# Kernel optimization log

Measured on AMD Instinct MI355X. Metric: run time of the kernel, lower is better.

The kernel has to match this reference:

```python
import jax, jax.numpy as jnp
import numpy as np

KH = KW = 3
K = KH * KW
GROUPS = 8


def conv_same(x, w, b=None):
    out = jax.lax.conv_general_dilated(x, w, (1, 1), 'SAME',
                                       dimension_numbers=('NHWC', 'HWIO', 'NHWC'))
    if b is not None:
        out = out + b
    return out


def feature_selection(x, w_att, w_sel):
    pooled = x.mean(axis=(1, 2), keepdims=True)            # [B,1,1,C]
    attn = jax.nn.sigmoid(conv_same(pooled, w_att))        # 1x1 conv, sigmoid
    return conv_same(x * (attn + 1.0), w_sel)              # [B,H,W,F]


def deform_sample(x, sy, sx):
    # x: [H,W,G,Cg]; sy,sx: [H,W,G,K] fractional sample coords (zero outside)
    H, W, G, _ = x.shape
    y0 = jnp.floor(sy)
    x0 = jnp.floor(sx)
    wy1 = sy - y0
    wx1 = sx - x0
    gi = jnp.arange(G)[None, None, :, None]

    def gather(yi, xi):
        valid = (yi >= 0) & (yi <= H - 1) & (xi >= 0) & (xi <= W - 1)
        yc = jnp.clip(yi, 0, H - 1).astype(jnp.int32)
        xc = jnp.clip(xi, 0, W - 1).astype(jnp.int32)
        v = x[yc, xc, gi]                                   # [H,W,G,K,Cg]
        return v * valid[..., None]

    v00 = gather(y0, x0)
    v01 = gather(y0, x0 + 1)
    v10 = gather(y0 + 1, x0)
    v11 = gather(y0 + 1, x0 + 1)
    wy1 = wy1[..., None]
    wx1 = wx1[..., None]
    top = v00 * (1 - wx1) + v01 * wx1
    bot = v10 * (1 - wx1) + v11 * wx1
    return top * (1 - wy1) + bot * wy1                      # [H,W,G,K,Cg]


def dcnv2(x, align, w_om, b_om, w_dcn, b_dcn):
    # x: [B,H,W,C] input to deform-conv; align: [B,H,W,Ca] alignment feature
    B, H, W, C = x.shape
    G = GROUPS
    Cg = C // G
    om = conv_same(align, w_om, b_om)                       # [B,H,W,G*3*K]
    off = om[..., :G * 2 * K].reshape(B, H, W, G, K, 2)     # (dy, dx)
    mask = jax.nn.sigmoid(om[..., G * 2 * K:]).reshape(B, H, W, G, K)

    iy = jnp.arange(H, dtype=x.dtype)[:, None, None, None]
    ix = jnp.arange(W, dtype=x.dtype)[None, :, None, None]
    ky, kx = jnp.meshgrid(jnp.arange(KH) - (KH - 1) // 2,
                          jnp.arange(KW) - (KW - 1) // 2, indexing='ij')
    ky = ky.reshape(K).astype(x.dtype)
    kx = kx.reshape(K).astype(x.dtype)
    sy = iy + ky + off[..., 0]                              # [B,H,W,G,K]
    sx = ix + kx + off[..., 1]

    xg = x.reshape(B, H, W, G, Cg)
    sampled = jax.vmap(deform_sample)(xg, sy, sx)           # [B,H,W,G,K,Cg]
    sampled = sampled * mask[..., None]
    sampled = sampled.transpose(0, 1, 2, 4, 3, 5).reshape(B, H, W, K, C)
    wk = w_dcn.reshape(K, C, -1)                            # [K,C,F]
    return jnp.einsum('bhwkc,kcf->bhwf', sampled, wk) + b_dcn


def reference(coarse, fine, w_att, w_sel, w_off, w_om, b_om, w_dcn, b_dcn):
    B, H, W, _ = fine.shape
    coarse_up = jax.image.resize(coarse, (B, H, W, coarse.shape[-1]), 'bilinear')
    fine_cal = feature_selection(fine, w_att, w_sel)
    fc = jnp.concatenate([fine_cal, coarse_up * 2.0], axis=-1)
    align = conv_same(fc, w_off)                            # 1x1, no bias
    aligned = jax.nn.relu(dcnv2(coarse_up, align, w_om, b_om, w_dcn, b_dcn))
    return aligned + fine_cal


def setup_inputs() -> dict:
    key = jax.random.key(0)
    ks = jax.random.split(key, 8)
    B, H, W = 4, 64, 64
    Cc, Cf, F = 256, 256, 256
    s = lambda fan: (2.0 / fan) ** 0.5
    return {
        'coarse': jax.random.normal(ks[0], (B, H // 2, W // 2, Cc), jnp.float32),
        'fine': jax.random.normal(ks[1], (B, H, W, Cf), jnp.float32),
        'w_att': jax.random.normal(ks[2], (1, 1, Cf, Cf), jnp.float32) * s(Cf),
        'w_sel': jax.random.normal(ks[3], (1, 1, Cf, F), jnp.float32) * s(Cf),
        'w_off': jax.random.normal(ks[4], (1, 1, F + Cc, 2 * F), jnp.float32) * s(F + Cc),
        'w_om': jax.random.normal(ks[5], (3, 3, 2 * F, GROUPS * 3 * K), jnp.float32) * 0.01,
        'b_om': jnp.zeros((GROUPS * 3 * K,), jnp.float32),
        'w_dcn': jax.random.normal(ks[6], (3, 3, Cc, F), jnp.float32) * s(9 * Cc),
        'b_dcn': jnp.zeros((F,), jnp.float32),
    }
```

## Files before the change

kernel.cpp:

```cpp
#include <hip/hip_runtime.h>
#include <hip/hip_bf16.h>
#include <cstddef>

constexpr int HWP = 64 * 64;
constexpr int CCH = 256;
constexpr int OMC = 216;
constexpr int KDC = 2304;

typedef __attribute__((ext_vector_type(8))) short bf16x8;
typedef __attribute__((ext_vector_type(4))) float f32x4;

__device__ inline unsigned short f2bf(float x) {
  __hip_bfloat16 h = __float2bfloat16(x);
  return *reinterpret_cast<unsigned short*>(&h);
}
__device__ inline float bf2f(unsigned short u) {
  unsigned int v = ((unsigned int)u) << 16;
  return __uint_as_float(v);
}
__device__ inline void bfpair(unsigned int u, float& a, float& b) {
  a = __uint_as_float(u << 16);
  b = __uint_as_float(u & 0xffff0000u);
}

__global__ __launch_bounds__(256) void prep_weights(
    const float* __restrict__ w_off, const float* __restrict__ w_om,
    const float* __restrict__ w_sel, const float* __restrict__ w_dcn,
    unsigned short* __restrict__ w_offT, unsigned short* __restrict__ w_omT,
    unsigned short* __restrict__ w_selT, unsigned short* __restrict__ w_dcnT) {
  int i = blockIdx.x * 256 + threadIdx.x;
  if (i < 512 * 512) {
    int n = i >> 9, k = i & 511;
    w_offT[i] = f2bf(w_off[k * 512 + n]);
  }
  if (i < 9 * 256 * 512) {
    int c = i & 511;
    int r = i >> 9;
    int tap = r >> 8;
    int n = r & 255;
    w_omT[i] = f2bf(n < OMC ? w_om[((size_t)tap * 512 + c) * OMC + n] : 0.f);
  }
  if (i < 256 * 256) {
    int n = i >> 8, k = i & 255;
    w_selT[i] = f2bf(w_sel[k * 256 + n]);
  }
  if (i < 9 * 256 * 256) {
    int tap = i >> 16, f = (i >> 8) & 255, c = i & 255;
    w_dcnT[i] = f2bf(w_dcn[((size_t)tap * 256 + c) * 256 + f]);
  }
}

__global__ __launch_bounds__(256) void pool_partial(
    const float* __restrict__ fine, float* __restrict__ partial) {
  int r = blockIdx.x;
  int b = blockIdx.y;
  int t = threadIdx.x;
  const float* src = fine + ((size_t)b * 4096 + r * 64) * 256 + t;
  float s = 0.f;
#pragma unroll 8
  for (int p = 0; p < 64; ++p) s += src[(size_t)p * 256];
  partial[((size_t)b * 64 + r) * 256 + t] = s;
}

__global__ __launch_bounds__(256) void pool_finish(
    const float* __restrict__ partial, const float* __restrict__ w_att,
    float* __restrict__ scale) {
  __shared__ float pl[256];
  int b = blockIdx.x;
  int t = threadIdx.x;
  const float* pp = partial + (size_t)b * 64 * 256 + t;
  float s = 0.f;
#pragma unroll 8
  for (int r = 0; r < 64; ++r) s += pp[(size_t)r * 256];
  pl[t] = s * (1.0f / 4096.0f);
  __syncthreads();
  float acc = 0.f;
  for (int ci = 0; ci < 256; ++ci) acc += pl[ci] * w_att[ci * 256 + t];
  scale[b * 256 + t] = 1.0f + 1.0f / (1.0f + expf(-acc));
}

__global__ __launch_bounds__(256) void upsample_kernel(
    const float* __restrict__ coarse, unsigned short* __restrict__ upbf,
    unsigned short* __restrict__ alignA) {
  int m = blockIdx.x;
  int c = threadIdx.x;
  int b = m >> 12, h = (m >> 6) & 63, w = m & 63;
  float cy = fminf(fmaxf(h * 0.5f - 0.25f, 0.f), 31.f);
  float cx = fminf(fmaxf(w * 0.5f - 0.25f, 0.f), 31.f);
  int y0 = (int)cy, x0 = (int)cx;
  float fy = cy - y0, fx = cx - x0;
  int y1 = min(y0 + 1, 31), x1 = min(x0 + 1, 31);
  const float* base = coarse + (size_t)b * 32 * 32 * CCH;
  float v00 = base[(y0 * 32 + x0) * CCH + c];
  float v01 = base[(y0 * 32 + x1) * CCH + c];
  float v10 = base[(y1 * 32 + x0) * CCH + c];
  float v11 = base[(y1 * 32 + x1) * CCH + c];
  float top = v00 + (v01 - v00) * fx;
  float bot = v10 + (v11 - v10) * fx;
  float v = top + (bot - top) * fy;
  upbf[(size_t)m * CCH + c] = f2bf(v);
  alignA[(size_t)m * 512 + 256 + c] = f2bf(2.f * v);
}

__global__ __launch_bounds__(256) void gemm_finecal_mfma(
    const float* __restrict__ fine, const float* __restrict__ scale,
    const unsigned short* __restrict__ w_selT,
    float* __restrict__ finecal, unsigned short* __restrict__ alignA) {
  __shared__ unsigned short As[128][72];
  __shared__ unsigned short Bs[64][72];
  __shared__ float sc[256];
  int n0 = blockIdx.x * 64;
  int m0 = blockIdx.y * 128;
  int t = threadIdx.x;
  int wid = t >> 6, lane = t & 63;
  int lrow = lane & 15, lq = lane >> 4;
  int bb = m0 >> 12;
  sc[t] = scale[bb * 256 + t];
  f32x4 acc[2][4];
#pragma unroll
  for (int i = 0; i < 2; ++i)
#pragma unroll
    for (int j = 0; j < 4; ++j) acc[i][j] = (f32x4){0.f, 0.f, 0.f, 0.f};
  for (int k0 = 0; k0 < 256; k0 += 64) {
    __syncthreads();
    for (int u = t; u < 128 * 8; u += 256) {
      int row = u >> 3, ck = u & 7;
      const float* fp = &fine[(size_t)(m0 + row) * 256 + k0 + ck * 8];
      float4 f0 = *(const float4*)fp;
      float4 f1 = *(const float4*)(fp + 4);
      int kb = k0 + ck * 8;
      ushort4 u0 = make_ushort4(f2bf(f0.x * sc[kb]), f2bf(f0.y * sc[kb + 1]),
                                f2bf(f0.z * sc[kb + 2]), f2bf(f0.w * sc[kb + 3]));
      ushort4 u1 = make_ushort4(f2bf(f1.x * sc[kb + 4]), f2bf(f1.y * sc[kb + 5]),
                                f2bf(f1.z * sc[kb + 6]), f2bf(f1.w * sc[kb + 7]));
      *(ushort4*)&As[row][ck * 8] = u0;
      *(ushort4*)&As[row][ck * 8 + 4] = u1;
    }
    for (int u = t; u < 64 * 8; u += 256) {
      int row = u >> 3, ck = u & 7;
      *(uint4*)&Bs[row][ck * 8] = *(const uint4*)&w_selT[(size_t)(n0 + row) * 256 + k0 + ck * 8];
    }
    __syncthreads();
#pragma unroll
    for (int kk = 0; kk < 2; ++kk) {
      bf16x8 a[2], b[4];
#pragma unroll
      for (int mt = 0; mt < 2; ++mt)
        a[mt] = *(const bf16x8*)&As[wid * 32 + mt * 16 + lrow][kk * 32 + lq * 8];
#pragma unroll
      for (int nt = 0; nt < 4; ++nt)
        b[nt] = *(const bf16x8*)&Bs[nt * 16 + lrow][kk * 32 + lq * 8];
#pragma unroll
      for (int mt = 0; mt < 2; ++mt)
#pragma unroll
        for (int nt = 0; nt < 4; ++nt)
          acc[mt][nt] = __builtin_amdgcn_mfma_f32_16x16x32_bf16(
              a[mt], b[nt], acc[mt][nt], 0, 0, 0);
    }
  }
#pragma unroll
  for (int mt = 0; mt < 2; ++mt)
#pragma unroll
    for (int nt = 0; nt < 4; ++nt)
#pragma unroll
      for (int r = 0; r < 4; ++r) {
        int m = m0 + wid * 32 + mt * 16 + lq * 4 + r;
        int n = n0 + nt * 16 + lrow;
        finecal[(size_t)m * 256 + n] = acc[mt][nt][r];
        alignA[(size_t)m * 512 + n] = f2bf(acc[mt][nt][r]);
      }
}

__global__ __launch_bounds__(256) void gemm_align_mfma(
    const unsigned short* __restrict__ alignA,
    const unsigned short* __restrict__ w_offT,
    unsigned short* __restrict__ alignBf) {
  __shared__ unsigned short As[128][72];
  __shared__ unsigned short Bs[64][72];
  int n0 = blockIdx.x * 64;
  int m0 = blockIdx.y * 128;
  int t = threadIdx.x;
  int wid = t >> 6, lane = t & 63;
  int lrow = lane & 15, lq = lane >> 4;
  f32x4 acc[2][4];
#pragma unroll
  for (int i = 0; i < 2; ++i)
#pragma unroll
    for (int j = 0; j < 4; ++j) acc[i][j] = (f32x4){0.f, 0.f, 0.f, 0.f};
  for (int k0 = 0; k0 < 512; k0 += 64) {
    __syncthreads();
    for (int u = t; u < 128 * 8; u += 256) {
      int row = u >> 3, ck = u & 7;
      *(uint4*)&As[row][ck * 8] =
          *(const uint4*)&alignA[(size_t)(m0 + row) * 512 + k0 + ck * 8];
    }
    for (int u = t; u < 64 * 8; u += 256) {
      int row = u >> 3, ck = u & 7;
      *(uint4*)&Bs[row][ck * 8] =
          *(const uint4*)&w_offT[(size_t)(n0 + row) * 512 + k0 + ck * 8];
    }
    __syncthreads();
#pragma unroll
    for (int kk = 0; kk < 2; ++kk) {
      bf16x8 a[2], b[4];
#pragma unroll
      for (int mt = 0; mt < 2; ++mt)
        a[mt] = *(const bf16x8*)&As[wid * 32 + mt * 16 + lrow][kk * 32 + lq * 8];
#pragma unroll
      for (int nt = 0; nt < 4; ++nt)
        b[nt] = *(const bf16x8*)&Bs[nt * 16 + lrow][kk * 32 + lq * 8];
#pragma unroll
      for (int mt = 0; mt < 2; ++mt)
#pragma unroll
        for (int nt = 0; nt < 4; ++nt)
          acc[mt][nt] = __builtin_amdgcn_mfma_f32_16x16x32_bf16(
              a[mt], b[nt], acc[mt][nt], 0, 0, 0);
    }
  }
#pragma unroll
  for (int mt = 0; mt < 2; ++mt)
#pragma unroll
    for (int nt = 0; nt < 4; ++nt)
#pragma unroll
      for (int r = 0; r < 4; ++r) {
        int m = m0 + wid * 32 + mt * 16 + lq * 4 + r;
        int n = n0 + nt * 16 + lrow;
        alignBf[(size_t)m * 512 + n] = f2bf(acc[mt][nt][r]);
      }
}

__global__ __launch_bounds__(256) void om_conv_mfma(
    const unsigned short* __restrict__ alignBf,
    const unsigned short* __restrict__ w_omT,
    const float* __restrict__ b_om,
    float* __restrict__ om) {
  __shared__ unsigned short As[4][66][72];
  __shared__ unsigned short Bs[2][64][72];
  int nblk = blockIdx.x;
  int mblk = blockIdx.y;
  int b = mblk >> 5, hp = mblk & 31;
  int h0 = hp * 2;
  int n0 = nblk * 64;
  int t = threadIdx.x;
  int wid = t >> 6, lane = t & 63;
  int wy = wid >> 1, wx = wid & 1;
  int lrow = lane & 15, lq = lane >> 4;
  const size_t imgbase = (size_t)b * 4096;
  f32x4 acc[4][2];
#pragma unroll
  for (int i = 0; i < 4; ++i)
#pragma unroll
    for (int j = 0; j < 2; ++j) acc[i][j] = (f32x4){0.f, 0.f, 0.f, 0.f};

  auto stageB = [&](int buf, int tap, int c0) {
    for (int u = t; u < 64 * 8; u += 256) {
      int n = u >> 3, ck = u & 7;
      *(uint4*)&Bs[buf][n][ck * 8] =
          *(const uint4*)&w_omT[((size_t)tap * 256 + n0 + n) * 512 + c0 * 64 + ck * 8];
    }
  };
  auto stageA = [&](int c0) {
    for (int u = t; u < 4 * 66 * 8; u += 256) {
      int dy = u / 528;
      int r = u - dy * 528;
      int px = r >> 3, ck = r & 7;
      int w = px - 1;
      int y = h0 - 1 + dy;
      uint4 v = make_uint4(0u, 0u, 0u, 0u);
      if (w >= 0 && w < 64 && y >= 0 && y < 64)
        v = *(const uint4*)&alignBf[(imgbase + y * 64 + w) * 512 + c0 * 64 + ck * 8];
      *(uint4*)&As[dy][px][ck * 8] = v;
    }
  };

  stageB(0, 0, 0);
  stageA(0);
  __syncthreads();
  int buf = 0;
  for (int c0 = 0; c0 < 8; ++c0) {
    for (int tap = 0; tap < 9; ++tap) {
      int ntap = tap + 1, nc0 = c0;
      if (ntap == 9) { ntap = 0; nc0 = (c0 + 1) & 7; }
      stageB(buf ^ 1, ntap, nc0);
      int dyt = tap / 3, dxt = tap - dyt * 3;
#pragma unroll
      for (int kk = 0; kk < 2; ++kk) {
        bf16x8 a[4], bb[2];
#pragma unroll
        for (int mt = 0; mt < 4; ++mt)
          a[mt] = *(const bf16x8*)&As[wy + dyt][mt * 16 + lrow + dxt][kk * 32 + lq * 8];
#pragma unroll
        for (int nt = 0; nt < 2; ++nt)
          bb[nt] = *(const bf16x8*)&Bs[buf][wx * 32 + nt * 16 + lrow][kk * 32 + lq * 8];
#pragma unroll
        for (int mt = 0; mt < 4; ++mt)
#pragma unroll
          for (int nt = 0; nt < 2; ++nt)
            acc[mt][nt] = __builtin_amdgcn_mfma_f32_16x16x32_bf16(
                a[mt], bb[nt], acc[mt][nt], 0, 0, 0);
      }
      __syncthreads();
      buf ^= 1;
    }
    if (c0 < 7) {
      stageA(c0 + 1);
      __syncthreads();
    }
  }
#pragma unroll
  for (int nt = 0; nt < 2; ++nt) {
    int n = n0 + wx * 32 + nt * 16 + lrow;
    if (n < OMC) {
      float bias = b_om[n];
#pragma unroll
      for (int mt = 0; mt < 4; ++mt) {
#pragma unroll
        for (int r = 0; r < 4; ++r) {
          size_t m = imgbase + (size_t)(h0 + wy) * 64 + mt * 16 + lq * 4 + r;
          om[m * OMC + n] = acc[mt][nt][r] + bias;
        }
      }
    }
  }
}

__global__ __launch_bounds__(256) void dcn_sample(
    const float* __restrict__ om, const unsigned short* __restrict__ upbf,
    unsigned short* __restrict__ S, int bh0) {
  __shared__ int offsA[256][4];
  __shared__ float wtsA[256][4];
  int blk = blockIdx.x;
  int bh = bh0 + (blk >> 1);
  int half = blk & 1;
  int b = bh >> 6, h = bh & 63;
  int p0 = half * 32;
  int m0g = bh * 64 + p0;
  int mloc0 = (bh - bh0) * 64 + p0;
  int t = threadIdx.x;
  const unsigned short* upb = upbf + (size_t)b * HWP * CCH;
  int lane = t & 63;
  int ph = t >> 6;
  int c = lane * 4;
  int g = lane >> 3;
  for (int tap = 0; tap < 9; ++tap) {
    int ky = tap / 3, kx = tap - ky * 3;
    __syncthreads();
    {
      int p = t >> 3, gg = t & 7;
      const float* omr = om + (size_t)(m0g + p) * OMC;
      float dy = omr[gg * 18 + tap * 2];
      float dx = omr[gg * 18 + tap * 2 + 1];
      float mk = 1.0f / (1.0f + expf(-omr[144 + gg * 9 + tap]));
      float sy = (float)(h + ky - 1) + dy;
      float sx = (float)(p0 + p + kx - 1) + dx;
      float y0f = floorf(sy), x0f = floorf(sx);
      float fy = sy - y0f, fx = sx - x0f;
      int y0 = (int)y0f, x0 = (int)x0f;
      int y1 = y0 + 1, x1 = x0 + 1;
      float vy0 = (y0 >= 0 && y0 <= 63) ? 1.f : 0.f;
      float vy1 = (y1 >= 0 && y1 <= 63) ? 1.f : 0.f;
      float vx0 = (x0 >= 0 && x0 <= 63) ? 1.f : 0.f;
      float vx1 = (x1 >= 0 && x1 <= 63) ? 1.f : 0.f;
      int yc0 = min(max(y0, 0), 63), yc1 = min(max(y1, 0), 63);
      int xc0 = min(max(x0, 0), 63), xc1 = min(max(x1, 0), 63);
      offsA[t][0] = (yc0 * 64 + xc0) * 256;
      offsA[t][1] = (yc0 * 64 + xc1) * 256;
      offsA[t][2] = (yc1 * 64 + xc0) * 256;
      offsA[t][3] = (yc1 * 64 + xc1) * 256;
      wtsA[t][0] = (1.f - fy) * (1.f - fx) * vy0 * vx0 * mk;
      wtsA[t][1] = (1.f - fy) * fx * vy0 * vx1 * mk;
      wtsA[t][2] = fy * (1.f - fx) * vy1 * vx0 * mk;
      wtsA[t][3] = fy * fx * vy1 * vx1 * mk;
    }
    __syncthreads();
#pragma unroll
    for (int pp = 0; pp < 8; ++pp) {
      int p = ph * 8 + pp;
      int idx = (p << 3) | g;
      int4 o = *(const int4*)&offsA[idx][0];
      float4 wv = *(const float4*)&wtsA[idx][0];
      uint2 u00 = *(const uint2*)&upb[o.x + c];
      uint2 u01 = *(const uint2*)&upb[o.y + c];
      uint2 u10 = *(const uint2*)&upb[o.z + c];
      uint2 u11 = *(const uint2*)&upb[o.w + c];
      float a0, a1, a2, a3, b0, b1, b2, b3, c0, c1, c2, c3, d0, d1, d2, d3;
      bfpair(u00.x, a0, a1); bfpair(u00.y, a2, a3);
      bfpair(u01.x, b0, b1); bfpair(u01.y, b2, b3);
      bfpair(u10.x, c0, c1); bfpair(u10.y, c2, c3);
      bfpair(u11.x, d0, d1); bfpair(u11.y, d2, d3);
      float v0 = wv.x * a0 + wv.y * b0 + wv.z * c0 + wv.w * d0;
      float v1 = wv.x * a1 + wv.y * b1 + wv.z * c1 + wv.w * d1;
      float v2 = wv.x * a2 + wv.y * b2 + wv.z * c2 + wv.w * d2;
      float v3 = wv.x * a3 + wv.y * b3 + wv.z * c3 + wv.w * d3;
      uint2 outv;
      outv.x = (unsigned int)f2bf(v0) | ((unsigned int)f2bf(v1) << 16);
      outv.y = (unsigned int)f2bf(v2) | ((unsigned int)f2bf(v3) << 16);
      *(uint2*)&S[(size_t)(mloc0 + p) * KDC + tap * 256 + c] = outv;
    }
  }
}

__global__ __launch_bounds__(256) void dcn_gemm(
    const unsigned short* __restrict__ S,
    const unsigned short* __restrict__ w_dcnT,
    const float* __restrict__ b_dcn,
    const float* __restrict__ finecal,
    float* __restrict__ outp, int m_base) {
  __shared__ unsigned short As[128][72];
  __shared__ unsigned short Bs[128][72];
  int n0 = blockIdx.x * 128;
  int mloc0 = blockIdx.y * 128;
  int m0 = m_base + mloc0;
  int t = threadIdx.x;
  int wid = t >> 6, lane = t & 63;
  int wy = wid >> 1, wx = wid & 1;
  int lrow = lane & 15, lq = lane >> 4;
  f32x4 acc[4][4];
#pragma unroll
  for (int i = 0; i < 4; ++i)
#pragma unroll
    for (int j = 0; j < 4; ++j) acc[i][j] = (f32x4){0.f, 0.f, 0.f, 0.f};
  for (int k0 = 0; k0 < KDC; k0 += 64) {
    __syncthreads();
    for (int u = t; u < 128 * 8; u += 256) {
      int row = u >> 3, ck = u & 7;
      *(uint4*)&As[row][ck * 8] =
          *(const uint4*)&S[(size_t)(mloc0 + row) * KDC + k0 + ck * 8];
    }
    int tap = k0 >> 8, c0 = k0 & 255;
    for (int u = t; u < 128 * 8; u += 256) {
      int row = u >> 3, ck = u & 7;
      *(uint4*)&Bs[row][ck * 8] =
          *(const uint4*)&w_dcnT[((size_t)tap * 256 + n0 + row) * 256 + c0 + ck * 8];
    }
    __syncthreads();
#pragma unroll
    for (int kk = 0; kk < 2; ++kk) {
      bf16x8 a[4], b[4];
#pragma unroll
      for (int mt = 0; mt < 4; ++mt)
        a[mt] = *(const bf16x8*)&As[wy * 64 + mt * 16 + lrow][kk * 32 + lq * 8];
#pragma unroll
      for (int nt = 0; nt < 4; ++nt)
        b[nt] = *(const bf16x8*)&Bs[wx * 64 + nt * 16 + lrow][kk * 32 + lq * 8];
#pragma unroll
      for (int mt = 0; mt < 4; ++mt)
#pragma unroll
        for (int nt = 0; nt < 4; ++nt)
          acc[mt][nt] = __builtin_amdgcn_mfma_f32_16x16x32_bf16(
              a[mt], b[nt], acc[mt][nt], 0, 0, 0);
    }
  }
#pragma unroll
  for (int mt = 0; mt < 4; ++mt)
#pragma unroll
    for (int nt = 0; nt < 4; ++nt) {
      int f = n0 + wx * 64 + nt * 16 + lrow;
      float bias = b_dcn[f];
#pragma unroll
      for (int r = 0; r < 4; ++r) {
        int m = m0 + wy * 64 + mt * 16 + lq * 4 + r;
        float v = fmaxf(acc[mt][nt][r] + bias, 0.f);
        float fc = __builtin_nontemporal_load(&finecal[(size_t)m * 256 + f]);
        __builtin_nontemporal_store(v + fc, &outp[(size_t)m * 256 + f]);
      }
    }
}

extern "C" void kernel_launch(void* const* d_in, const int* in_sizes, int n_in,
                              void* d_out, int out_size, void* d_ws, size_t ws_size,
                              hipStream_t stream) {
  const float* coarse = (const float*)d_in[0];
  const float* fine   = (const float*)d_in[1];
  const float* w_att  = (const float*)d_in[2];
  const float* w_sel  = (const float*)d_in[3];
  const float* w_off  = (const float*)d_in[4];
  const float* w_om   = (const float*)d_in[5];
  const float* b_om   = (const float*)d_in[6];
  const float* w_dcn  = (const float*)d_in[7];
  const float* b_dcn  = (const float*)d_in[8];
  float* outp = (float*)d_out;

  char* base = (char*)d_ws;
  size_t o = 0;
  float* scale            = (float*)(base + o);          o += 4096;
  float* finecal          = (float*)(base + o);          o += 16777216;
  float* omb              = (float*)(base + o);          o += 14155776;
  unsigned short* upbf    = (unsigned short*)(base + o); o += 8388608;
  unsigned short* w_offT  = (unsigned short*)(base + o); o += 524288;
  unsigned short* w_omT   = (unsigned short*)(base + o); o += 2359296;
  unsigned short* w_selT  = (unsigned short*)(base + o); o += 131072;
  unsigned short* w_dcnT  = (unsigned short*)(base + o); o += 1179648;
  unsigned short* Sbuf    = (unsigned short*)(base + o);
  size_t fixed = o;
  unsigned short* alignA  = Sbuf;
  unsigned short* alignBf = (unsigned short*)((char*)Sbuf + 16777216);
  float* partial = omb;

  bool fullS = (ws_size >= fixed + 75497472);

  prep_weights<<<dim3(4608), dim3(256), 0, stream>>>(
      w_off, w_om, w_sel, w_dcn, w_offT, w_omT, w_selT, w_dcnT);
  pool_partial<<<dim3(64, 4), dim3(256), 0, stream>>>(fine, partial);
  pool_finish<<<dim3(4), dim3(256), 0, stream>>>(partial, w_att, scale);
  upsample_kernel<<<dim3(16384), dim3(256), 0, stream>>>(coarse, upbf, alignA);
  gemm_finecal_mfma<<<dim3(4, 128), dim3(256), 0, stream>>>(
      fine, scale, w_selT, finecal, alignA);
  gemm_align_mfma<<<dim3(8, 128), dim3(256), 0, stream>>>(alignA, w_offT, alignBf);
  om_conv_mfma<<<dim3(4, 128), dim3(256), 0, stream>>>(alignBf, w_omT, b_om, omb);

  if (fullS) {
    dcn_sample<<<dim3(512), dim3(256), 0, stream>>>(omb, upbf, Sbuf, 0);
    dcn_gemm<<<dim3(2, 128), dim3(256), 0, stream>>>(
        Sbuf, w_dcnT, b_dcn, finecal, outp, 0);
  } else {
    for (int ch = 0; ch < 2; ++ch) {
      dcn_sample<<<dim3(256), dim3(256), 0, stream>>>(omb, upbf, Sbuf, ch * 128);
      dcn_gemm<<<dim3(2, 64), dim3(256), 0, stream>>>(
          Sbuf, w_dcnT, b_dcn, finecal, outp, ch * 8192);
    }
  }
}
```

Baseline: 443.3 us.

## Double-buffer LDS tiles in dcn_gemm with register prefetch of next K slice

The DCN GEMM kernel now keeps two LDS buffers for the A and B tiles. Each thread loads the next K slice into registers before the MFMA work on the current slice, then stores it into the other buffer afterwards. This cuts the loop to one barrier per iteration and lets global-load latency overlap the matrix math. In exchange it doubles LDS use to about 73KB per block, which can lower occupancy, and adds prefetch registers.

Result: faster. 424.0 us (-4.4%).

```diff
diff --git a/kernel.cpp b/kernel.cpp
--- a/kernel.cpp
+++ b/kernel.cpp
@@ -405,9 +405,9 @@
     const unsigned short* __restrict__ w_dcnT,
     const float* __restrict__ b_dcn,
     const float* __restrict__ finecal,
-    float* __restrict__ outp, int m_base) {
-  __shared__ unsigned short As[128][72];
-  __shared__ unsigned short Bs[128][72];
+    float* __restrict__ outp, int m_base, int kiters) {
+  __shared__ unsigned short As[2][128][72];
+  __shared__ unsigned short Bs[2][128][72];
   int n0 = blockIdx.x * 128;
   int mloc0 = blockIdx.y * 128;
   int m0 = m_base + mloc0;
@@ -420,35 +420,60 @@
   for (int i = 0; i < 4; ++i)
 #pragma unroll
     for (int j = 0; j < 4; ++j) acc[i][j] = (f32x4){0.f, 0.f, 0.f, 0.f};
-  for (int k0 = 0; k0 < KDC; k0 += 64) {
-    __syncthreads();
-    for (int u = t; u < 128 * 8; u += 256) {
-      int row = u >> 3, ck = u & 7;
-      *(uint4*)&As[row][ck * 8] =
-          *(const uint4*)&S[(size_t)(mloc0 + row) * KDC + k0 + ck * 8];
-    }
+
+  int arow = t >> 3, ack = t & 7;
+  uint4 pa[4], pb[4];
+  auto loadA = [&](int k0, uint4* p) {
+#pragma unroll
+    for (int i = 0; i < 4; ++i)
+      p[i] = *(const uint4*)&S[(size_t)(mloc0 + arow + i * 32) * KDC + k0 + ack * 8];
+  };
+  auto loadB = [&](int k0, uint4* p) {
     int tap = k0 >> 8, c0 = k0 & 255;
-    for (int u = t; u < 128 * 8; u += 256) {
-      int row = u >> 3, ck = u & 7;
-      *(uint4*)&Bs[row][ck * 8] =
-          *(const uint4*)&w_dcnT[((size_t)tap * 256 + n0 + row) * 256 + c0 + ck * 8];
-    }
-    __syncthreads();
+#pragma unroll
+    for (int i = 0; i < 4; ++i)
+      p[i] = *(const uint4*)&w_dcnT[((size_t)tap * 256 + n0 + arow + i * 32) * 256 + c0 + ack * 8];
+  };
+  auto storeTiles = [&](int buf, const uint4* a, const uint4* b) {
+#pragma unroll
+    for (int i = 0; i < 4; ++i)
+      *(uint4*)&As[buf][arow + i * 32][ack * 8] = a[i];
+#pragma unroll
+    for (int i = 0; i < 4; ++i)
+      *(uint4*)&Bs[buf][arow + i * 32][ack * 8] = b[i];
+  };
+
+  loadA(0, pa);
+  loadB(0, pb);
+  storeTiles(0, pa, pb);
+  __syncthreads();
+  int buf = 0;
+  for (int kb = 0; kb < kiters; ++kb) {
+    bool has_next = (kb + 1) < kiters;
+    if (has_next) {
+      loadA((kb + 1) * 64, pa);
+      loadB((kb + 1) * 64, pb);
+    }
 #pragma unroll
     for (int kk = 0; kk < 2; ++kk) {
       bf16x8 a[4], b[4];
 #pragma unroll
       for (int mt = 0; mt < 4; ++mt)
-        a[mt] = *(const bf16x8*)&As[wy * 64 + mt * 16 + lrow][kk * 32 + lq * 8];
+        a[mt] = *(const bf16x8*)&As[buf][wy * 64 + mt * 16 + lrow][kk * 32 + lq * 8];
 #pragma unroll
       for (int nt = 0; nt < 4; ++nt)
-        b[nt] = *(const bf16x8*)&Bs[wx * 64 + nt * 16 + lrow][kk * 32 + lq * 8];
+        b[nt] = *(const bf16x8*)&Bs[buf][wx * 64 + nt * 16 + lrow][kk * 32 + lq * 8];
 #pragma unroll
       for (int mt = 0; mt < 4; ++mt)
 #pragma unroll
         for (int nt = 0; nt < 4; ++nt)
           acc[mt][nt] = __builtin_amdgcn_mfma_f32_16x16x32_bf16(
               a[mt], b[nt], acc[mt][nt], 0, 0, 0);
+    }
+    if (has_next) {
+      storeTiles(buf ^ 1, pa, pb);
+      __syncthreads();
+      buf ^= 1;
     }
   }
 #pragma unroll
@@ -512,12 +537,12 @@
   if (fullS) {
     dcn_sample<<<dim3(512), dim3(256), 0, stream>>>(omb, upbf, Sbuf, 0);
     dcn_gemm<<<dim3(2, 128), dim3(256), 0, stream>>>(
-        Sbuf, w_dcnT, b_dcn, finecal, outp, 0);
+        Sbuf, w_dcnT, b_dcn, finecal, outp, 0, KDC / 64);
   } else {
     for (int ch = 0; ch < 2; ++ch) {
       dcn_sample<<<dim3(256), dim3(256), 0, stream>>>(omb, upbf, Sbuf, ch * 128);
       dcn_gemm<<<dim3(2, 64), dim3(256), 0, stream>>>(
-          Sbuf, w_dcnT, b_dcn, finecal, outp, ch * 8192);
-    }
-  }
-}
+          Sbuf, w_dcnT, b_dcn, finecal, outp, ch * 8192, KDC / 64);
+    }
+  }
+}
```
